# Kernel optimization log

Hardware: AMD Instinct MI355X
Metric: run time of the kernel (lower is better)

Reference implementation:

```python
import jax, jax.numpy as jnp
import numpy as np

B, S, T = 2048, 32, 32
D, H = 128, 256       # cle_dim, rnn_dim
VS, VT = 256, 256     # source/target char vocab
BOW = 1               # MorphoDataset.Factor.BOW


def setup_inputs() -> dict:
    key = jax.random.key(0)
    ks = jax.random.split(key, 16)
    n = lambda k, sh: (jax.random.normal(k, sh, jnp.float32) * 0.05)
    inp = {
        "src_emb": n(ks[0], (VS, D)),
        "tgt_emb": n(ks[1], (VT, D)),
        "enc_f_W": n(ks[2], (D, 3 * H)),
        "enc_f_U": n(ks[3], (H, 3 * H)),
        "enc_f_b": jnp.zeros((2, 3 * H), jnp.float32),
        "enc_b_W": n(ks[4], (D, 3 * H)),
        "enc_b_U": n(ks[5], (H, 3 * H)),
        "enc_b_b": jnp.zeros((2, 3 * H), jnp.float32),
        "dec_W": n(ks[6], (D + H, 3 * H)),
        "dec_U": n(ks[7], (H, 3 * H)),
        "dec_b": jnp.zeros((2, 3 * H), jnp.float32),
        "out_W": n(ks[8], (H, VT)),
        "out_b": jnp.zeros((VT,), jnp.float32),
        "att_src_W": n(ks[9], (H, H)),
        "att_src_b": jnp.zeros((H,), jnp.float32),
        "att_st_W": n(ks[10], (H, H)),
        "att_st_b": jnp.zeros((H,), jnp.float32),
        "att_v": n(ks[11], (H, 1)),
        "att_v_b": jnp.zeros((1,), jnp.float32),
        "source_ids": jax.random.randint(ks[12], (B, S), 0, VS, jnp.int32),
        "target_ids": jax.random.randint(ks[13], (B, T), 0, VT, jnp.int32),
    }
    return inp


def _gru_step(h, x, W, U, b):
    # Keras GRU, reset_after=True: separate input/recurrent biases b[0], b[1]
    gx = x @ W + b[0]
    gh = h @ U + b[1]
    xz, xr, xh = jnp.split(gx, 3, axis=-1)
    hz, hr, hh = jnp.split(gh, 3, axis=-1)
    z = jax.nn.sigmoid(xz + hz)
    r = jax.nn.sigmoid(xr + hr)
    c = jnp.tanh(xh + r * hh)
    return z * h + (1.0 - z) * c


def _gru_scan(x_tbd, W, U, b):
    # x_tbd: [S, B, D] -> outputs [S, B, H]
    h0 = jnp.zeros((x_tbd.shape[1], U.shape[0]), x_tbd.dtype)
    def step(h, x):
        h = _gru_step(h, x, W, U, b)
        return h, h
    _, ys = jax.lax.scan(step, h0, x_tbd)
    return ys


def reference(src_emb, tgt_emb, enc_f_W, enc_f_U, enc_f_b, enc_b_W, enc_b_U, enc_b_b,
              dec_W, dec_U, dec_b, out_W, out_b, att_src_W, att_src_b,
              att_st_W, att_st_b, att_v, att_v_b, source_ids, target_ids):
    # ---- Encoder: bidirectional GRU, merge_mode='sum' ----
    x = src_emb[source_ids]                      # [B, S, D]
    x_t = jnp.transpose(x, (1, 0, 2))            # [S, B, D]
    fwd = _gru_scan(x_t, enc_f_W, enc_f_U, enc_f_b)
    bwd = _gru_scan(x_t[::-1], enc_b_W, enc_b_U, enc_b_b)[::-1]
    source_states = jnp.transpose(fwd + bwd, (1, 0, 2))  # [B, S, H]

    # projected source states are constant across decoder steps -> precompute
    proj_src = source_states @ att_src_W + att_src_b     # [B, S, H]

    def attend(inp, h):
        p = h @ att_st_W + att_st_b                      # [B, H]
        e = jnp.tanh(proj_src + p[:, None, :]) @ att_v + att_v_b  # [B, S, 1]
        w = jax.nn.softmax(e, axis=1)                    # softmax over source positions
        ctx = jnp.sum(source_states * w, axis=1)         # [B, H]
        return jnp.concatenate([inp, ctx], axis=1)       # [B, D+H]

    # ---- Decoder (teacher forcing) ----
    h0 = source_states[:, 0]                             # [B, H]
    bow = jnp.broadcast_to(tgt_emb[BOW], (source_ids.shape[0], tgt_emb.shape[1]))
    inp0 = attend(bow, h0)

    def dstep(carry, tgt_t):
        h, inp = carry
        h = _gru_step(h, inp, dec_W, dec_U, dec_b)       # GRUCell step
        logits = h @ out_W + out_b                       # [B, VT]
        nxt = attend(tgt_emb[tgt_t], h)
        return (h, nxt), logits

    _, logits = jax.lax.scan(dstep, (h0, inp0), jnp.transpose(target_ids))
    return jnp.transpose(logits, (1, 0, 2))              # [B, T, VT]
```

## Files before the change

### kernel.cpp

```cpp
#include <hip/hip_runtime.h>
#include <math.h>

#define B_  2048
#define S_  32
#define T_  32
#define D_  128
#define H_  256
#define G3  768
#define VT_ 256
#define BOW_ 1

typedef __attribute__((ext_vector_type(8))) short short8;
typedef __attribute__((ext_vector_type(4))) float f32x4;
typedef __attribute__((ext_vector_type(8))) unsigned short us8;
typedef unsigned short u16;

__device__ inline u16 f2bf(float x) {
  union { float f; unsigned u; } v; v.f = x;
  unsigned r = v.u + 0x7FFFu + ((v.u >> 16) & 1u);
  return (u16)(r >> 16);
}
__device__ inline float bf2f(u16 b) {
  union { unsigned u; float f; } v; v.u = ((unsigned)b) << 16; return v.f;
}
__device__ inline int swz(int r) { return ((r ^ (r >> 3)) & 7) << 3; }
__device__ inline float sigm(float x) { return 1.f / (1.f + expf(-x)); }

struct TMat { const float* src; u16* dhi; u16* dlo; int R; int C; int tile0; };
struct TPack { TMat m[10]; };

__global__ __launch_bounds__(256)
void wsplit_t(TPack P) {
  int bx = blockIdx.x;
  TMat M = P.m[0];
  #pragma unroll
  for (int i = 1; i < 10; i++) if (bx >= P.m[i].tile0) M = P.m[i];
  int ti = bx - M.tile0;
  int tilesR = M.R >> 6;
  int rt = ti % tilesR, ct = ti / tilesR;
  int r0 = rt * 64, c0 = ct * 64;
  __shared__ float ts[64][65];
  int tid = threadIdx.x;
  int cx = tid & 63, ry = tid >> 6;
  #pragma unroll
  for (int i = 0; i < 16; i++) {
    int r = ry * 16 + i;
    ts[r][cx] = M.src[(size_t)(r0 + r) * M.C + c0 + cx];
  }
  __syncthreads();
  int rx = tid & 63, cy = tid >> 6;
  #pragma unroll
  for (int i = 0; i < 16; i++) {
    int cc = cy * 16 + i;
    float v = ts[rx][cc];
    u16 hi = f2bf(v);
    size_t o = (size_t)(c0 + cc) * M.R + r0 + rx;
    M.dhi[o] = hi;
    M.dlo[o] = f2bf(v - bf2f(hi));
  }
}

__global__ __launch_bounds__(256)
void esplit(const float* a, const float* b, u16* ah, u16* al, u16* bh, u16* bl, int n) {
  int i = blockIdx.x * 256 + threadIdx.x;
  if (i >= 2 * n) return;
  const float* s = (i < n) ? a : b;
  u16* dh = (i < n) ? ah : bh;
  u16* dl = (i < n) ? al : bl;
  int j = (i < n) ? i : i - n;
  float v = s[j];
  u16 hi = f2bf(v);
  dh[j] = hi; dl[j] = f2bf(v - bf2f(hi));
}

struct PLeg {
  const u16* Ahi; const u16* Alo; int lda;
  const u16* Bthi; const u16* Btlo; int ldb;
  const float* bias; void* C; int ldc; int cmode;
  int M, N, K;
};

__global__ __launch_bounds__(256)
void gemm_pl(PLeg l0, PLeg l1) {
  PLeg L = blockIdx.z ? l1 : l0;
  int n0 = blockIdx.x * 128; if (n0 >= L.N) return;
  int m0 = blockIdx.y * 128; if (m0 >= L.M) return;
  __shared__ u16 As[128 * 64];
  __shared__ u16 Bs[128 * 64];
  int tid = threadIdx.x;
  int lane = tid & 63, wv = tid >> 6;
  int wr = (wv >> 1) * 64, wc = (wv & 1) * 64;
  int fr = lane & 15, fk = (lane >> 4) * 8;
  f32x4 acc[4][4];
  #pragma unroll
  for (int m = 0; m < 4; m++)
    #pragma unroll
    for (int n = 0; n < 4; n++) acc[m][n] = (f32x4){0.f, 0.f, 0.f, 0.f};

  int s_row = tid >> 1, s_part = tid & 1;

  for (int k0 = 0; k0 < L.K; k0 += 32) {
    if (k0) __syncthreads();
    int swA = swz(s_row);
    {
      const u16* src = (s_part ? L.Alo : L.Ahi) + (size_t)(m0 + s_row) * L.lda + k0;
      #pragma unroll
      for (int q = 0; q < 4; q++)
        *(us8*)&As[(s_row * 64 + s_part * 32 + q * 8) ^ swA] = *(const us8*)(src + q * 8);
    }
    {
      const u16* src = (s_part ? L.Btlo : L.Bthi) + (size_t)(n0 + s_row) * L.ldb + k0;
      #pragma unroll
      for (int q = 0; q < 4; q++)
        *(us8*)&Bs[(s_row * 64 + s_part * 32 + q * 8) ^ swA] = *(const us8*)(src + q * 8);
    }
    __syncthreads();
    short8 bhi[4], blo[4];
    #pragma unroll
    for (int n = 0; n < 4; n++) {
      int cc = wc + n * 16 + fr; int sw = swz(cc);
      bhi[n] = *(const short8*)&Bs[(cc * 64 + fk) ^ sw];
      blo[n] = *(const short8*)&Bs[(cc * 64 + 32 + fk) ^ sw];
    }
    #pragma unroll
    for (int m = 0; m < 4; m++) {
      int r = wr + m * 16 + fr; int sw = swz(r);
      short8 ahi = *(const short8*)&As[(r * 64 + fk) ^ sw];
      short8 alo = *(const short8*)&As[(r * 64 + 32 + fk) ^ sw];
      #pragma unroll
      for (int n = 0; n < 4; n++) {
        acc[m][n] = __builtin_amdgcn_mfma_f32_16x16x32_bf16(ahi, bhi[n], acc[m][n], 0, 0, 0);
        acc[m][n] = __builtin_amdgcn_mfma_f32_16x16x32_bf16(ahi, blo[n], acc[m][n], 0, 0, 0);
        acc[m][n] = __builtin_amdgcn_mfma_f32_16x16x32_bf16(alo, bhi[n], acc[m][n], 0, 0, 0);
      }
    }
  }
  int rbase = (lane >> 4) * 4;
  #pragma unroll
  for (int m = 0; m < 4; m++)
    #pragma unroll
    for (int rr = 0; rr < 4; rr++) {
      int row = m0 + wr + m * 16 + rbase + rr;
      #pragma unroll
      for (int n = 0; n < 4; n++) {
        int col = n0 + wc + n * 16 + fr;
        float v = acc[m][n][rr];
        if (L.bias) v += L.bias[col];
        if (L.cmode == 0)      ((float*)L.C)[(size_t)row * L.ldc + col] = v;
        else if (L.cmode == 1) ((u16*)L.C)[(size_t)row * L.ldc + col] = f2bf(v);
        else {
          size_t o = (((size_t)(row & (B_ - 1))) * T_ + (row >> 11)) * VT_ + col;
          ((float*)L.C)[o] = v;
        }
      }
    }
}

struct GruDesc {
  const u16 *a0H, *a0L;
  const u16 *a1H, *a1L;
  const u16 *b0H, *b0L;
  const u16 *b1H, *b1L;
  const float *gxT;
  const float *bias0, *bias1;
  const float *hold;
  const u16 *holdH, *holdL;
  float *hnew;
  u16 *hh, *hl;
  u16 *ssH, *ssL;
  const int *ids;
  int ssmode;
  int sidx, rev;
};

template<int MODE>
__global__ __launch_bounds__(256)
void gru_step(GruDesc d0, GruDesc d1) {
  GruDesc D = blockIdx.z ? d1 : d0;
  constexpr int KT  = MODE ? 512 : 256;
  constexpr int KT8 = KT / 8;
  constexpr int MF  = MODE ? 1 : 2;
  constexpr int NST = KT / 32;
  __shared__ __align__(16) u16 As[2 * 32 * KT];

  int m0 = blockIdx.y * 32;
  int tid = threadIdx.x;
  int lane = tid & 63, wv = tid >> 6;
  int fr = lane & 15, kq = lane >> 4;
  int jn, rb0;
  if (MODE == 0) { jn = blockIdx.x * 64 + wv * 16 + fr; rb0 = 0; }
  else           { jn = blockIdx.x * 32 + (wv & 1) * 16 + fr; rb0 = (wv >> 1) * 16; }

  constexpr int PER_T = (2 * 32 * KT8) / 256;
  #pragma unroll
  for (int i = 0; i < PER_T; i++) {
    int s = tid + i * 256;
    int p = s / (32 * KT8);
    int rem = s - p * (32 * KT8);
    int row = rem / KT8;
    int kb = rem - row * KT8;
    int k = kb * 8;
    const u16* src;
    if (MODE == 0) {
      src = (p ? D.a0L : D.a0H) + (size_t)(m0 + row) * 256 + k;
    } else {
      src = (k < 256) ? (p ? D.a0L : D.a0H) + (size_t)(m0 + row) * 256 + k
                      : (p ? D.a1L : D.a1H) + (size_t)(m0 + row) * 256 + (k - 256);
    }
    *(us8*)&As[(s ^ (row & 7)) * 8] = *(const us8*)src;
  }
  __syncthreads();

  f32x4 acc[4][MF];
  #pragma unroll
  for (int a = 0; a < 4; a++)
    #pragma unroll
    for (int mf = 0; mf < MF; mf++) acc[a][mf] = (f32x4){0.f, 0.f, 0.f, 0.f};

  #pragma unroll
  for (int i = 0; i < NST; i++) {
    const u16 *BH, *BL; int bk, ai2;
    if (MODE == 0)    { BH = D.b0H; BL = D.b0L; bk = i * 32; ai2 = 2; }
    else if (i < 8)   { BH = D.b0H; BL = D.b0L; bk = i * 32; ai2 = 2; }
    else              { BH = D.b1H; BL = D.b1L; bk = (i - 8) * 32; ai2 = 3; }
    short8 ah[MF], al[MF];
    #pragma unroll
    for (int mf = 0; mf < MF; mf++) {
      int rp = rb0 + mf * 16 + fr;
      int kb = i * 4 + kq;
      ah[mf] = *(const short8*)&As[((rp * KT8 + kb) ^ (fr & 7)) * 8];
      al[mf] = *(const short8*)&As[((32 * KT8 + rp * KT8 + kb) ^ (fr & 7)) * 8];
    }
    #pragma unroll
    for (int st = 0; st < 3; st++) {
      size_t ro = (size_t)(st * 256 + jn) * 256 + bk + kq * 8;
      short8 bh = *(const short8*)(BH + ro);
      short8 bl = *(const short8*)(BL + ro);
      int ai = (st < 2) ? st : ai2;
      #pragma unroll
      for (int mf = 0; mf < MF; mf++) {
        acc[ai][mf] = __builtin_amdgcn_mfma_f32_16x16x32_bf16(ah[mf], bh, acc[ai][mf], 0, 0, 0);
        acc[ai][mf] = __builtin_amdgcn_mfma_f32_16x16x32_bf16(ah[mf], bl, acc[ai][mf], 0, 0, 0);
        acc[ai][mf] = __builtin_amdgcn_mfma_f32_16x16x32_bf16(al[mf], bh, acc[ai][mf], 0, 0, 0);
      }
    }
  }

  int rbase = kq * 4;
  int j = jn;
  float b0z = D.bias0[j],       b1z = D.bias1[j];
  float b0r = D.bias0[256 + j], b1r = D.bias1[256 + j];
  float b0c = D.bias0[512 + j], b1c = D.bias1[512 + j];
  #pragma unroll
  for (int mf = 0; mf < MF; mf++)
    #pragma unroll
    for (int rr = 0; rr < 4; rr++) {
      int b = m0 + rb0 + mf * 16 + rbase + rr;
      size_t o = (size_t)b * H_ + j;
      int id;
      if (MODE == 0) id = D.ids[b * S_ + (D.rev ? (S_ - 1 - D.sidx) : D.sidx)];
      else           id = (D.sidx == 0) ? BOW_ : D.ids[b * T_ + D.sidx - 1];
      const float* T = D.gxT + (size_t)id * G3;
      float z = sigm(acc[0][mf][rr] + T[j] + b0z + b1z);
      float r = sigm(acc[1][mf][rr] + T[256 + j] + b0r + b1r);
      float xc = T[512 + j] + b0c + (MODE ? acc[3][mf][rr] : 0.f);
      float c = tanhf(xc + r * (acc[2][mf][rr] + b1c));
      float hprev = D.hold ? D.hold[o] : (bf2f(D.holdH[o]) + bf2f(D.holdL[o]));
      float hn = z * hprev + (1.f - z) * c;
      D.hnew[o] = hn;
      u16 hi = f2bf(hn);
      D.hh[o] = hi; D.hl[o] = f2bf(hn - bf2f(hi));
      if (MODE == 0) {
        if (D.ssmode == 1) {
          D.ssH[o] = hi; D.ssL[o] = f2bf(hn - bf2f(hi));
        } else if (D.ssmode == 2) {
          float v = bf2f(D.ssH[o]) + bf2f(D.ssL[o]) + hn;
          u16 vh = f2bf(v);
          D.ssH[o] = vh; D.ssL[o] = f2bf(v - bf2f(vh));
        }
      }
    }
}

__global__ __launch_bounds__(256)
void attend_k(const u16* __restrict__ projbf, const u16* __restrict__ ssH,
              const float* __restrict__ p, const float* __restrict__ att_v,
              u16* __restrict__ ctxh, u16* __restrict__ ctxl) {
  int b = blockIdx.x;
  int tid = threadIdx.x;
  int lane = tid & 63;
  int wv = tid >> 6;
  __shared__ float e_s[S_];
  __shared__ float w_s[S_];
  float pq[4], vq[4];
  #pragma unroll
  for (int q = 0; q < 4; q++) {
    pq[q] = p[(size_t)b * H_ + q * 64 + lane];
    vq[q] = att_v[q * 64 + lane];
  }
  float pv[8][4];
  #pragma unroll
  for (int i = 0; i < 8; i++) {
    const u16* pr = projbf + ((size_t)(wv * 8 + i) * B_ + b) * H_;
    #pragma unroll
    for (int q = 0; q < 4; q++) pv[i][q] = bf2f(pr[q * 64 + lane]);
  }
  u16 sv[S_];
  #pragma unroll
  for (int s = 0; s < S_; s++) sv[s] = ssH[((size_t)s * B_ + b) * H_ + tid];

  #pragma unroll
  for (int i = 0; i < 8; i++) {
    float part = 0.f;
    #pragma unroll
    for (int q = 0; q < 4; q++)
      part += tanhf(pv[i][q] + pq[q]) * vq[q];
    #pragma unroll
    for (int off = 32; off; off >>= 1)
      part += __shfl_xor(part, off);
    if (lane == 0) e_s[wv * 8 + i] = part;
  }
  __syncthreads();
  float m = -1e30f;
  #pragma unroll
  for (int s = 0; s < S_; s++) m = fmaxf(m, e_s[s]);
  float den = 0.f;
  #pragma unroll
  for (int s = 0; s < S_; s++) den += expf(e_s[s] - m);
  if (tid < S_) w_s[tid] = expf(e_s[tid] - m) / den;
  __syncthreads();
  float acc = 0.f;
  #pragma unroll
  for (int s = 0; s < S_; s++)
    acc = fmaf(w_s[s], bf2f(sv[s]), acc);
  u16 hi = f2bf(acc);
  size_t o = (size_t)b * H_ + tid;
  ctxh[o] = hi; ctxl[o] = f2bf(acc - bf2f(hi));
}

extern "C" void kernel_launch(void* const* d_in, const int* in_sizes, int n_in,
                              void* d_out, int out_size, void* d_ws, size_t ws_size,
                              hipStream_t stream) {
  const float* src_emb   = (const float*)d_in[0];
  const float* tgt_emb   = (const float*)d_in[1];
  const float* enc_f_W   = (const float*)d_in[2];
  const float* enc_f_U   = (const float*)d_in[3];
  const float* enc_f_b   = (const float*)d_in[4];
  const float* enc_b_W   = (const float*)d_in[5];
  const float* enc_b_U   = (const float*)d_in[6];
  const float* enc_b_b   = (const float*)d_in[7];
  const float* dec_W     = (const float*)d_in[8];
  const float* dec_U     = (const float*)d_in[9];
  const float* dec_b     = (const float*)d_in[10];
  const float* out_W     = (const float*)d_in[11];
  const float* out_b     = (const float*)d_in[12];
  const float* att_src_W = (const float*)d_in[13];
  const float* att_src_b = (const float*)d_in[14];
  const float* att_st_W  = (const float*)d_in[15];
  const float* att_st_b  = (const float*)d_in[16];
  const float* att_v     = (const float*)d_in[17];
  const int* source_ids  = (const int*)d_in[19];
  const int* target_ids  = (const int*)d_in[20];
  float* out = (float*)d_out;

  char* base = (char*)d_ws;
  size_t off = 0;
  auto allocB = [&](size_t bytes) { void* p = base + off; off = (off + bytes + 255) & ~255UL; return p; };
  const size_t BH = (size_t)B_ * H_;

  u16* ssH    = (u16*)allocB((size_t)S_ * BH * 2);
  u16* ssL    = (u16*)allocB((size_t)S_ * BH * 2);
  u16* projbf = (u16*)allocB((size_t)S_ * BH * 2);
  float* pbuf = (float*)allocB(BH * 4);
  u16* ctxh = (u16*)allocB(BH * 2);
  u16* ctxl = (u16*)allocB(BH * 2);

  float* encF0 = (float*)allocB(2 * BH * 4);
  u16*  encPl0 = (u16*)allocB(4 * BH * 2);
  float* encF1 = (float*)allocB(2 * BH * 4);
  u16*  encPl1 = (u16*)allocB(4 * BH * 2);
  float* encF[2][2]  = { { encF0, encF0 + BH }, { encF1, encF1 + BH } };
  u16*  encH[2][2]   = { { encPl0, encPl0 + 2 * BH }, { encPl1, encPl1 + 2 * BH } };
  u16*  encL[2][2]   = { { encPl0 + BH, encPl0 + 3 * BH }, { encPl1 + BH, encPl1 + 3 * BH } };

  float* hDecF[2] = { (float*)allocB(BH * 4), (float*)allocB(BH * 4) };
  u16* hAllH = (u16*)allocB((size_t)T_ * BH * 2);
  u16* hAllL = (u16*)allocB((size_t)T_ * BH * 2);

  auto planes2 = [&](size_t n, u16*& h, u16*& l) { h = (u16*)allocB(n * 2); l = (u16*)allocB(n * 2); };
  u16 *UtFh,*UtFl,*UtBh,*UtBl,*WtFh,*WtFl,*WtBh,*WtBl;
  u16 *dUth,*dUtl,*dWcth,*dWctl,*dWxth,*dWxtl;
  u16 *oWth,*oWtl,*aStth,*aSttl,*aSrth,*aSrtl;
  u16 *sEh,*sEl,*tEh,*tEl;
  planes2((size_t)G3*H_, UtFh, UtFl);   planes2((size_t)G3*H_, UtBh, UtBl);
  planes2((size_t)G3*D_, WtFh, WtFl);   planes2((size_t)G3*D_, WtBh, WtBl);
  planes2((size_t)G3*H_, dUth, dUtl);   planes2((size_t)G3*H_, dWcth, dWctl);
  planes2((size_t)G3*D_, dWxth, dWxtl);
  planes2((size_t)H_*VT_, oWth, oWtl);
  planes2((size_t)H_*H_, aSrth, aSrtl);
  planes2((size_t)H_*H_, aStth, aSttl);
  planes2((size_t)VT_*D_, sEh, sEl);    planes2((size_t)VT_*D_, tEh, tEl);
  float* Tf = (float*)allocB((size_t)VT_ * G3 * 4);
  float* Tb = (float*)allocB((size_t)VT_ * G3 * 4);
  float* Td = (float*)allocB((size_t)VT_ * G3 * 4);

  TPack P;
  P.m[0] = { enc_f_U,          UtFh, UtFl, 256, 768, 0   };
  P.m[1] = { enc_b_U,          UtBh, UtBl, 256, 768, 48  };
  P.m[2] = { dec_U,            dUth, dUtl, 256, 768, 96  };
  P.m[3] = { dec_W + 128 * G3, dWcth, dWctl, 256, 768, 144 };
  P.m[4] = { enc_f_W,          WtFh, WtFl, 128, 768, 192 };
  P.m[5] = { enc_b_W,          WtBh, WtBl, 128, 768, 216 };
  P.m[6] = { dec_W,            dWxth, dWxtl, 128, 768, 240 };
  P.m[7] = { out_W,            oWth, oWtl, 256, 256, 264 };
  P.m[8] = { att_src_W,        aSrth, aSrtl, 256, 256, 280 };
  P.m[9] = { att_st_W,         aStth, aSttl, 256, 256, 296 };
  wsplit_t<<<312, 256, 0, stream>>>(P);
  esplit<<<(2 * VT_ * D_ + 255) / 256, 256, 0, stream>>>(src_emb, tgt_emb, sEh, sEl, tEh, tEl, VT_ * D_);

  {
    PLeg tf = { sEh, sEl, D_, WtFh, WtFl, D_, nullptr, Tf, G3, 0, VT_, G3, D_ };
    PLeg tb = { sEh, sEl, D_, WtBh, WtBl, D_, nullptr, Tb, G3, 0, VT_, G3, D_ };
    gemm_pl<<<dim3(6, 2, 2), 256, 0, stream>>>(tf, tb);
    PLeg td = { tEh, tEl, D_, dWxth, dWxtl, D_, nullptr, Td, G3, 0, VT_, G3, D_ };
    gemm_pl<<<dim3(6, 2, 1), 256, 0, stream>>>(td, td);
  }

  hipMemsetAsync(encF0, 0, 2 * BH * 4, stream);
  hipMemsetAsync(encPl0, 0, 4 * BH * 2, stream);

  for (int s = 0; s < S_; s++) {
    int p = s & 1;
    GruDesc dd[2];
    for (int d = 0; d < 2; d++) {
      GruDesc& D = dd[d];
      D.a0H = encH[p][d]; D.a0L = encL[p][d];
      D.a1H = nullptr; D.a1L = nullptr;
      D.b0H = d ? UtBh : UtFh; D.b0L = d ? UtBl : UtFl;
      D.b1H = nullptr; D.b1L = nullptr;
      D.gxT = d ? Tb : Tf;
      D.bias0 = d ? enc_b_b : enc_f_b;
      D.bias1 = (d ? enc_b_b : enc_f_b) + G3;
      D.hold = encF[p][d]; D.holdH = nullptr; D.holdL = nullptr;
      D.hnew = encF[p ^ 1][d];
      D.hh = encH[p ^ 1][d]; D.hl = encL[p ^ 1][d];
      int pos = d ? (S_ - 1 - s) : s;
      D.ssH = ssH + (size_t)pos * BH; D.ssL = ssL + (size_t)pos * BH;
      D.ids = source_ids;
      D.ssmode = (s < S_ / 2) ? 1 : 2;
      D.sidx = s; D.rev = d;
    }
    gru_step<0><<<dim3(4, 64, 2), 256, 0, stream>>>(dd[0], dd[1]);
  }

  {
    PLeg proj = { ssH, ssL, H_, aSrth, aSrtl, H_, att_src_b, projbf, H_, 1, S_ * B_, H_, H_ };
    PLeg p0   = { ssH, ssL, H_, aStth, aSttl, H_, att_st_b,  pbuf,   H_, 0, B_,      H_, H_ };
    gemm_pl<<<dim3(2, 512, 2), 256, 0, stream>>>(proj, p0);
  }
  attend_k<<<B_, 256, 0, stream>>>(projbf, ssH, pbuf, att_v, ctxh, ctxl);

  for (int t = 0; t < T_; t++) {
    int p = t & 1;
    GruDesc D = {};
    D.a0H = t ? hAllH + (size_t)(t - 1) * BH : ssH;
    D.a0L = t ? hAllL + (size_t)(t - 1) * BH : ssL;
    D.a1H = ctxh; D.a1L = ctxl;
    D.b0H = dUth;  D.b0L = dUtl;
    D.b1H = dWcth; D.b1L = dWctl;
    D.gxT = Td;
    D.bias0 = dec_b; D.bias1 = dec_b + G3;
    if (t == 0) { D.hold = nullptr; D.holdH = ssH; D.holdL = ssL; }
    else        { D.hold = hDecF[p]; D.holdH = nullptr; D.holdL = nullptr; }
    D.hnew = hDecF[p ^ 1];
    D.hh = hAllH + (size_t)t * BH; D.hl = hAllL + (size_t)t * BH;
    D.ssH = nullptr; D.ssL = nullptr;
    D.ids = target_ids;
    D.ssmode = 0; D.sidx = t; D.rev = 0;
    gru_step<1><<<dim3(8, 64, 1), 256, 0, stream>>>(D, D);

    if (t < T_ - 1) {
      PLeg LP = { hAllH + (size_t)t * BH, hAllL + (size_t)t * BH, H_,
                  aStth, aSttl, H_, att_st_b, pbuf, H_, 0, B_, H_, H_ };
      gemm_pl<<<dim3(2, 16, 1), 256, 0, stream>>>(LP, LP);
      attend_k<<<B_, 256, 0, stream>>>(projbf, ssH, pbuf, att_v, ctxh, ctxl);
    }
  }

  {
    PLeg LO = { hAllH, hAllL, H_, oWth, oWtl, H_, out_b, out, 0, 2, T_ * B_, VT_, H_ };
    gemm_pl<<<dim3(2, 512, 1), 256, 0, stream>>>(LO, LO);
  }
}
```

Baseline: 3.604 ms.

## Fuse decoder GRU step, attention projection and attention into one kernel

Replaces the per-timestep decoder sequence of GRU kernel, state-projection GEMM and attention kernel with a single dec_step kernel. Each 512-thread block owns 8 batch rows: it computes the GRU update, projects the new state through att_st_W, and computes the attention context, with intermediates kept in shared memory. This removes two launches per step and the global round trip of the projected state. In exchange, every block streams the full recurrent and attention weights, and the 8-row tiles are padded to the 16-row MFMA shape, so half of the matrix work is wasted. The encoder GRU kernel is also specialised into its own non-templated version with fixed indexing.

```diff
diff --git a/kernel.cpp b/kernel.cpp
--- a/kernel.cpp
+++ b/kernel.cpp
@@ -14,6 +14,8 @@
 typedef __attribute__((ext_vector_type(4))) float f32x4;
 typedef __attribute__((ext_vector_type(8))) unsigned short us8;
 typedef unsigned short u16;
+
+#define MFMA16 __builtin_amdgcn_mfma_f32_16x16x32_bf16
 
 __device__ inline u16 f2bf(float x) {
   union { float f; unsigned u; } v; v.f = x;
@@ -129,9 +131,9 @@
       short8 alo = *(const short8*)&As[(r * 64 + 32 + fk) ^ sw];
       #pragma unroll
       for (int n = 0; n < 4; n++) {
-        acc[m][n] = __builtin_amdgcn_mfma_f32_16x16x32_bf16(ahi, bhi[n], acc[m][n], 0, 0, 0);
-        acc[m][n] = __builtin_amdgcn_mfma_f32_16x16x32_bf16(ahi, blo[n], acc[m][n], 0, 0, 0);
-        acc[m][n] = __builtin_amdgcn_mfma_f32_16x16x32_bf16(alo, bhi[n], acc[m][n], 0, 0, 0);
+        acc[m][n] = MFMA16(ahi, bhi[n], acc[m][n], 0, 0, 0);
+        acc[m][n] = MFMA16(ahi, blo[n], acc[m][n], 0, 0, 0);
+        acc[m][n] = MFMA16(alo, bhi[n], acc[m][n], 0, 0, 0);
       }
     }
   }
@@ -156,15 +158,12 @@
     }
 }
 
-struct GruDesc {
+struct EncD {
   const u16 *a0H, *a0L;
-  const u16 *a1H, *a1L;
   const u16 *b0H, *b0L;
-  const u16 *b1H, *b1L;
   const float *gxT;
   const float *bias0, *bias1;
   const float *hold;
-  const u16 *holdH, *holdL;
   float *hnew;
   u16 *hh, *hl;
   u16 *ssH, *ssL;
@@ -173,111 +172,89 @@
   int sidx, rev;
 };
 
-template<int MODE>
 __global__ __launch_bounds__(256)
-void gru_step(GruDesc d0, GruDesc d1) {
-  GruDesc D = blockIdx.z ? d1 : d0;
-  constexpr int KT  = MODE ? 512 : 256;
-  constexpr int KT8 = KT / 8;
-  constexpr int MF  = MODE ? 1 : 2;
-  constexpr int NST = KT / 32;
-  __shared__ __align__(16) u16 As[2 * 32 * KT];
+void enc_step(EncD d0, EncD d1) {
+  EncD D = blockIdx.z ? d1 : d0;
+  __shared__ __align__(16) u16 As[2 * 32 * 256];
 
   int m0 = blockIdx.y * 32;
   int tid = threadIdx.x;
   int lane = tid & 63, wv = tid >> 6;
   int fr = lane & 15, kq = lane >> 4;
-  int jn, rb0;
-  if (MODE == 0) { jn = blockIdx.x * 64 + wv * 16 + fr; rb0 = 0; }
-  else           { jn = blockIdx.x * 32 + (wv & 1) * 16 + fr; rb0 = (wv >> 1) * 16; }
-
-  constexpr int PER_T = (2 * 32 * KT8) / 256;
-  #pragma unroll
-  for (int i = 0; i < PER_T; i++) {
+  int jn = blockIdx.x * 64 + wv * 16 + fr;
+
+  #pragma unroll
+  for (int i = 0; i < 8; i++) {
     int s = tid + i * 256;
-    int p = s / (32 * KT8);
-    int rem = s - p * (32 * KT8);
-    int row = rem / KT8;
-    int kb = rem - row * KT8;
-    int k = kb * 8;
-    const u16* src;
-    if (MODE == 0) {
-      src = (p ? D.a0L : D.a0H) + (size_t)(m0 + row) * 256 + k;
-    } else {
-      src = (k < 256) ? (p ? D.a0L : D.a0H) + (size_t)(m0 + row) * 256 + k
-                      : (p ? D.a1L : D.a1H) + (size_t)(m0 + row) * 256 + (k - 256);
-    }
+    int p = s >> 10;
+    int rem = s & 1023;
+    int row = rem >> 5;
+    const u16* src = (p ? D.a0L : D.a0H) + (size_t)(m0 + row) * 256 + (rem & 31) * 8;
     *(us8*)&As[(s ^ (row & 7)) * 8] = *(const us8*)src;
   }
   __syncthreads();
 
-  f32x4 acc[4][MF];
-  #pragma unroll
-  for (int a = 0; a < 4; a++)
-    #pragma unroll
-    for (int mf = 0; mf < MF; mf++) acc[a][mf] = (f32x4){0.f, 0.f, 0.f, 0.f};
-
-  #pragma unroll
-  for (int i = 0; i < NST; i++) {
-    const u16 *BH, *BL; int bk, ai2;
-    if (MODE == 0)    { BH = D.b0H; BL = D.b0L; bk = i * 32; ai2 = 2; }
-    else if (i < 8)   { BH = D.b0H; BL = D.b0L; bk = i * 32; ai2 = 2; }
-    else              { BH = D.b1H; BL = D.b1L; bk = (i - 8) * 32; ai2 = 3; }
-    short8 ah[MF], al[MF];
-    #pragma unroll
-    for (int mf = 0; mf < MF; mf++) {
-      int rp = rb0 + mf * 16 + fr;
+  f32x4 acc[3];
+  #pragma unroll
+  for (int a = 0; a < 3; a++) acc[a] = (f32x4){0.f,0.f,0.f,0.f};
+  f32x4 acc2[3];
+  #pragma unroll
+  for (int a = 0; a < 3; a++) acc2[a] = (f32x4){0.f,0.f,0.f,0.f};
+
+  #pragma unroll
+  for (int i = 0; i < 8; i++) {
+    short8 ah[2], al[2];
+    #pragma unroll
+    for (int mf = 0; mf < 2; mf++) {
+      int rp = mf * 16 + fr;
       int kb = i * 4 + kq;
-      ah[mf] = *(const short8*)&As[((rp * KT8 + kb) ^ (fr & 7)) * 8];
-      al[mf] = *(const short8*)&As[((32 * KT8 + rp * KT8 + kb) ^ (fr & 7)) * 8];
+      ah[mf] = *(const short8*)&As[((rp * 32 + kb) ^ (fr & 7)) * 8];
+      al[mf] = *(const short8*)&As[((1024 + rp * 32 + kb) ^ (fr & 7)) * 8];
     }
     #pragma unroll
     for (int st = 0; st < 3; st++) {
-      size_t ro = (size_t)(st * 256 + jn) * 256 + bk + kq * 8;
-      short8 bh = *(const short8*)(BH + ro);
-      short8 bl = *(const short8*)(BL + ro);
-      int ai = (st < 2) ? st : ai2;
-      #pragma unroll
-      for (int mf = 0; mf < MF; mf++) {
-        acc[ai][mf] = __builtin_amdgcn_mfma_f32_16x16x32_bf16(ah[mf], bh, acc[ai][mf], 0, 0, 0);
-        acc[ai][mf] = __builtin_amdgcn_mfma_f32_16x16x32_bf16(ah[mf], bl, acc[ai][mf], 0, 0, 0);
-        acc[ai][mf] = __builtin_amdgcn_mfma_f32_16x16x32_bf16(al[mf], bh, acc[ai][mf], 0, 0, 0);
-      }
-    }
-  }
-
+      size_t ro = (size_t)(st * 256 + jn) * 256 + i * 32 + kq * 8;
+      short8 bh = *(const short8*)(D.b0H + ro);
+      short8 bl = *(const short8*)(D.b0L + ro);
+      acc[st]  = MFMA16(ah[0], bh, acc[st], 0, 0, 0);
+      acc[st]  = MFMA16(ah[0], bl, acc[st], 0, 0, 0);
+      acc[st]  = MFMA16(al[0], bh, acc[st], 0, 0, 0);
+      acc2[st] = MFMA16(ah[1], bh, acc2[st], 0, 0, 0);
+      acc2[st] = MFMA16(ah[1], bl, acc2[st], 0, 0, 0);
+      acc2[st] = MFMA16(al[1], bh, acc2[st], 0, 0, 0);
+    }
+  }
+
+  float b0z = D.bias0[jn] + D.bias1[jn];
+  float b0r = D.bias0[256 + jn] + D.bias1[256 + jn];
+  float bxc = D.bias0[512 + jn];
+  float bhc = D.bias1[512 + jn];
   int rbase = kq * 4;
-  int j = jn;
-  float b0z = D.bias0[j],       b1z = D.bias1[j];
-  float b0r = D.bias0[256 + j], b1r = D.bias1[256 + j];
-  float b0c = D.bias0[512 + j], b1c = D.bias1[512 + j];
-  #pragma unroll
-  for (int mf = 0; mf < MF; mf++)
+  #pragma unroll
+  for (int mf = 0; mf < 2; mf++)
     #pragma unroll
     for (int rr = 0; rr < 4; rr++) {
-      int b = m0 + rb0 + mf * 16 + rbase + rr;
-      size_t o = (size_t)b * H_ + j;
-      int id;
-      if (MODE == 0) id = D.ids[b * S_ + (D.rev ? (S_ - 1 - D.sidx) : D.sidx)];
-      else           id = (D.sidx == 0) ? BOW_ : D.ids[b * T_ + D.sidx - 1];
+      int b = m0 + mf * 16 + rbase + rr;
+      size_t o = (size_t)b * H_ + jn;
+      int id = D.ids[b * S_ + (D.rev ? (S_ - 1 - D.sidx) : D.sidx)];
       const float* T = D.gxT + (size_t)id * G3;
-      float z = sigm(acc[0][mf][rr] + T[j] + b0z + b1z);
-      float r = sigm(acc[1][mf][rr] + T[256 + j] + b0r + b1r);
-      float xc = T[512 + j] + b0c + (MODE ? acc[3][mf][rr] : 0.f);
-      float c = tanhf(xc + r * (acc[2][mf][rr] + b1c));
-      float hprev = D.hold ? D.hold[o] : (bf2f(D.holdH[o]) + bf2f(D.holdL[o]));
-      float hn = z * hprev + (1.f - z) * c;
+      float az  = mf ? acc2[0][rr] : acc[0][rr];
+      float ar  = mf ? acc2[1][rr] : acc[1][rr];
+      float ahc = mf ? acc2[2][rr] : acc[2][rr];
+      float z = sigm(az + T[jn] + b0z);
+      float r = sigm(ar + T[256 + jn] + b0r);
+      float c = tanhf(T[512 + jn] + bxc + r * (ahc + bhc));
+      float hn = z * D.hold[o] + (1.f - z) * c;
       D.hnew[o] = hn;
       u16 hi = f2bf(hn);
-      D.hh[o] = hi; D.hl[o] = f2bf(hn - bf2f(hi));
-      if (MODE == 0) {
-        if (D.ssmode == 1) {
-          D.ssH[o] = hi; D.ssL[o] = f2bf(hn - bf2f(hi));
-        } else if (D.ssmode == 2) {
-          float v = bf2f(D.ssH[o]) + bf2f(D.ssL[o]) + hn;
-          u16 vh = f2bf(v);
-          D.ssH[o] = vh; D.ssL[o] = f2bf(v - bf2f(vh));
-        }
+      u16 lo = f2bf(hn - bf2f(hi));
+      D.hh[o] = hi; D.hl[o] = lo;
+      if (D.ssmode == 1) {
+        D.ssH[o] = hi; D.ssL[o] = lo;
+      } else {
+        float v = bf2f(D.ssH[o]) + bf2f(D.ssL[o]) + hn;
+        u16 vh = f2bf(v);
+        D.ssH[o] = vh; D.ssL[o] = f2bf(v - bf2f(vh));
       }
     }
 }
@@ -336,6 +313,195 @@
   u16 hi = f2bf(acc);
   size_t o = (size_t)b * H_ + tid;
   ctxh[o] = hi; ctxl[o] = f2bf(acc - bf2f(hi));
+}
+
+struct DSP {
+  const u16 *hPH, *hPL;
+  const float *hPF;
+  float *hFo;
+  const u16 *UH, *UL, *CH, *CL;
+  const u16 *sWH, *sWL;
+  const float *gxT, *bias, *stb, *attv;
+  const u16 *ssH;
+  const u16 *projbf;
+  u16 *hAH, *hAL;
+  u16 *ctxH, *ctxL;
+  const int *ids;
+  int t, last;
+};
+
+__global__ __launch_bounds__(512, 1)
+void dec_step(DSP P) {
+  __shared__ __align__(16) u16 AH[16 * 512];
+  __shared__ __align__(16) u16 AL[16 * 512];
+  __shared__ float pS[8 * 256];
+  const int tid = threadIdx.x;
+  const int lane = tid & 63, w = tid >> 6;
+  const int fr = lane & 15, kq = lane >> 4;
+  const int r0 = blockIdx.x * 8;
+
+  #pragma unroll
+  for (int i = 0; i < 4; i++) {
+    int s = tid + i * 512;
+    int p = s >> 10;
+    int rem = s & 1023;
+    int row = rem >> 6;
+    int k8 = rem & 63;
+    us8 v = {0,0,0,0,0,0,0,0};
+    if (row < 8) {
+      const u16* src = (k8 < 32)
+        ? (p ? P.hPL : P.hPH) + (size_t)(r0 + row) * 256 + k8 * 8
+        : (p ? P.ctxL : P.ctxH) + (size_t)(r0 + row) * 256 + (k8 - 32) * 8;
+      v = *(const us8*)src;
+    }
+    int slot = row * 64 + (k8 ^ (row & 7));
+    if (p) *(us8*)&AL[slot * 8] = v;
+    else   *(us8*)&AH[slot * 8] = v;
+  }
+  __syncthreads();
+
+  f32x4 acc[4][2];
+  #pragma unroll
+  for (int a = 0; a < 4; a++)
+    #pragma unroll
+    for (int q = 0; q < 2; q++) acc[a][q] = (f32x4){0.f,0.f,0.f,0.f};
+
+  #pragma unroll
+  for (int i = 0; i < 16; i++) {
+    int slot = fr * 64 + ((i * 4 + kq) ^ (fr & 7));
+    short8 ah = *(const short8*)&AH[slot * 8];
+    short8 al = *(const short8*)&AL[slot * 8];
+    const u16* BH = (i < 8) ? P.UH : P.CH;
+    const u16* BL = (i < 8) ? P.UL : P.CL;
+    int bk = (i & 7) * 32 + kq * 8;
+    int ci = (i < 8) ? 2 : 3;
+    #pragma unroll
+    for (int st = 0; st < 3; st++) {
+      int ai = (st < 2) ? st : ci;
+      #pragma unroll
+      for (int q = 0; q < 2; q++) {
+        size_t ro = (size_t)(st * 256 + (2 * w + q) * 16 + fr) * 256 + bk;
+        short8 bh = *(const short8*)(BH + ro);
+        short8 bl = *(const short8*)(BL + ro);
+        acc[ai][q] = MFMA16(ah, bh, acc[ai][q], 0, 0, 0);
+        acc[ai][q] = MFMA16(ah, bl, acc[ai][q], 0, 0, 0);
+        acc[ai][q] = MFMA16(al, bh, acc[ai][q], 0, 0, 0);
+      }
+    }
+  }
+  __syncthreads();
+
+  if (kq < 2) {
+    #pragma unroll
+    for (int rr = 0; rr < 4; rr++) {
+      int row = kq * 4 + rr;
+      int gb = r0 + row;
+      int id = (P.t == 0) ? BOW_ : P.ids[gb * T_ + P.t - 1];
+      const float* T = P.gxT + (size_t)id * G3;
+      #pragma unroll
+      for (int q = 0; q < 2; q++) {
+        int j = (2 * w + q) * 16 + fr;
+        size_t o = (size_t)gb * H_ + j;
+        float z = sigm(acc[0][q][rr] + T[j] + P.bias[j] + P.bias[G3 + j]);
+        float r = sigm(acc[1][q][rr] + T[256 + j] + P.bias[256 + j] + P.bias[G3 + 256 + j]);
+        float c = tanhf(T[512 + j] + P.bias[512 + j] + acc[3][q][rr]
+                        + r * (acc[2][q][rr] + P.bias[G3 + 512 + j]));
+        float hp;
+        if (P.hPF) hp = P.hPF[o];
+        else {
+          int sl = row * 64 + ((j >> 3) ^ (row & 7));
+          hp = bf2f(AH[sl * 8 + (j & 7)]) + bf2f(AL[sl * 8 + (j & 7)]);
+        }
+        float hn = z * hp + (1.f - z) * c;
+        P.hFo[o] = hn;
+        u16 hi = f2bf(hn);
+        u16 lo = f2bf(hn - bf2f(hi));
+        P.hAH[o] = hi; P.hAL[o] = lo;
+        int sl = row * 64 + ((j >> 3) ^ (row & 7));
+        AH[sl * 8 + (j & 7)] = hi;
+        AL[sl * 8 + (j & 7)] = lo;
+      }
+    }
+  }
+  if (P.last) return;
+  __syncthreads();
+
+  f32x4 pa[2];
+  #pragma unroll
+  for (int q = 0; q < 2; q++) pa[q] = (f32x4){0.f,0.f,0.f,0.f};
+  #pragma unroll
+  for (int i = 0; i < 8; i++) {
+    int slot = fr * 64 + ((i * 4 + kq) ^ (fr & 7));
+    short8 ah = *(const short8*)&AH[slot * 8];
+    short8 al = *(const short8*)&AL[slot * 8];
+    #pragma unroll
+    for (int q = 0; q < 2; q++) {
+      size_t ro = (size_t)((2 * w + q) * 16 + fr) * 256 + i * 32 + kq * 8;
+      short8 bh = *(const short8*)(P.sWH + ro);
+      short8 bl = *(const short8*)(P.sWL + ro);
+      pa[q] = MFMA16(ah, bh, pa[q], 0, 0, 0);
+      pa[q] = MFMA16(ah, bl, pa[q], 0, 0, 0);
+      pa[q] = MFMA16(al, bh, pa[q], 0, 0, 0);
+    }
+  }
+  if (kq < 2) {
+    #pragma unroll
+    for (int rr = 0; rr < 4; rr++) {
+      int row = kq * 4 + rr;
+      #pragma unroll
+      for (int q = 0; q < 2; q++) {
+        int j = (2 * w + q) * 16 + fr;
+        pS[row * 256 + j] = pa[q][rr] + P.stb[j];
+      }
+    }
+  }
+  __syncthreads();
+
+  {
+    int gb = r0 + w;
+    float pq[4], vq[4];
+    #pragma unroll
+    for (int q = 0; q < 4; q++) {
+      pq[q] = pS[w * 256 + q * 64 + lane];
+      vq[q] = P.attv[q * 64 + lane];
+    }
+    float sc[S_];
+    #pragma unroll 8
+    for (int s2 = 0; s2 < S_; s2++) {
+      const u16* pr = P.projbf + ((size_t)s2 * B_ + gb) * 256;
+      float part = 0.f;
+      #pragma unroll
+      for (int q = 0; q < 4; q++)
+        part += tanhf(bf2f(pr[q * 64 + lane]) + pq[q]) * vq[q];
+      #pragma unroll
+      for (int off = 32; off; off >>= 1)
+        part += __shfl_xor(part, off);
+      sc[s2] = part;
+    }
+    float m = -1e30f;
+    #pragma unroll
+    for (int s2 = 0; s2 < S_; s2++) m = fmaxf(m, sc[s2]);
+    float den = 0.f;
+    #pragma unroll
+    for (int s2 = 0; s2 < S_; s2++) { sc[s2] = expf(sc[s2] - m); den += sc[s2]; }
+    float inv = 1.f / den;
+    float cacc[4] = {0.f, 0.f, 0.f, 0.f};
+    #pragma unroll 8
+    for (int s2 = 0; s2 < S_; s2++) {
+      float wgt = sc[s2] * inv;
+      const u16* sp = P.ssH + ((size_t)s2 * B_ + gb) * 256;
+      #pragma unroll
+      for (int q = 0; q < 4; q++)
+        cacc[q] = fmaf(wgt, bf2f(sp[q * 64 + lane]), cacc[q]);
+    }
+    #pragma unroll
+    for (int q = 0; q < 4; q++) {
+      size_t o = (size_t)gb * H_ + q * 64 + lane;
+      u16 hi = f2bf(cacc[q]);
+      P.ctxH[o] = hi;
+      P.ctxL[o] = f2bf(cacc[q] - bf2f(hi));
+    }
+  }
 }
 
 extern "C" void kernel_launch(void* const* d_in, const int* in_sizes, int n_in,
@@ -431,17 +597,15 @@
 
   for (int s = 0; s < S_; s++) {
     int p = s & 1;
-    GruDesc dd[2];
+    EncD dd[2];
     for (int d = 0; d < 2; d++) {
-      GruDesc& D = dd[d];
+      EncD& D = dd[d];
       D.a0H = encH[p][d]; D.a0L = encL[p][d];
-      D.a1H = nullptr; D.a1L = nullptr;
       D.b0H = d ? UtBh : UtFh; D.b0L = d ? UtBl : UtFl;
-      D.b1H = nullptr; D.b1L = nullptr;
       D.gxT = d ? Tb : Tf;
       D.bias0 = d ? enc_b_b : enc_f_b;
       D.bias1 = (d ? enc_b_b : enc_f_b) + G3;
-      D.hold = encF[p][d]; D.holdH = nullptr; D.holdL = nullptr;
+      D.hold = encF[p][d];
       D.hnew = encF[p ^ 1][d];
       D.hh = encH[p ^ 1][d]; D.hl = encL[p ^ 1][d];
       int pos = d ? (S_ - 1 - s) : s;
@@ -450,7 +614,7 @@
       D.ssmode = (s < S_ / 2) ? 1 : 2;
       D.sidx = s; D.rev = d;
     }
-    gru_step<0><<<dim3(4, 64, 2), 256, 0, stream>>>(dd[0], dd[1]);
+    enc_step<<<dim3(4, 64, 2), 256, 0, stream>>>(dd[0], dd[1]);
   }
 
   {
@@ -461,30 +625,21 @@
   attend_k<<<B_, 256, 0, stream>>>(projbf, ssH, pbuf, att_v, ctxh, ctxl);
 
   for (int t = 0; t < T_; t++) {
-    int p = t & 1;
-    GruDesc D = {};
-    D.a0H = t ? hAllH + (size_t)(t - 1) * BH : ssH;
-    D.a0L = t ? hAllL + (size_t)(t - 1) * BH : ssL;
-    D.a1H = ctxh; D.a1L = ctxl;
-    D.b0H = dUth;  D.b0L = dUtl;
-    D.b1H = dWcth; D.b1L = dWctl;
-    D.gxT = Td;
-    D.bias0 = dec_b; D.bias1 = dec_b + G3;
-    if (t == 0) { D.hold = nullptr; D.holdH = ssH; D.holdL = ssL; }
-    else        { D.hold = hDecF[p]; D.holdH = nullptr; D.holdL = nullptr; }
-    D.hnew = hDecF[p ^ 1];
-    D.hh = hAllH + (size_t)t * BH; D.hl = hAllL + (size_t)t * BH;
-    D.ssH = nullptr; D.ssL = nullptr;
+    DSP D;
+    D.hPH = t ? hAllH + (size_t)(t - 1) * BH : ssH;
+    D.hPL = t ? hAllL + (size_t)(t - 1) * BH : ssL;
+    D.hPF = t ? hDecF[t & 1] : nullptr;
+    D.hFo = hDecF[(t & 1) ^ 1];
+    D.UH = dUth; D.UL = dUtl; D.CH = dWcth; D.CL = dWctl;
+    D.sWH = aStth; D.sWL = aSttl;
+    D.gxT = Td; D.bias = dec_b; D.stb = att_st_b; D.attv = att_v;
+    D.ssH = ssH;
+    D.projbf = projbf;
+    D.hAH = hAllH + (size_t)t * BH; D.hAL = hAllL + (size_t)t * BH;
+    D.ctxH = ctxh; D.ctxL = ctxl;
     D.ids = target_ids;
-    D.ssmode = 0; D.sidx = t; D.rev = 0;
-    gru_step<1><<<dim3(8, 64, 1), 256, 0, stream>>>(D, D);
-
-    if (t < T_ - 1) {
-      PLeg LP = { hAllH + (size_t)t * BH, hAllL + (size_t)t * BH, H_,
-                  aStth, aSttl, H_, att_st_b, pbuf, H_, 0, B_, H_, H_ };
-      gemm_pl<<<dim3(2, 16, 1), 256, 0, stream>>>(LP, LP);
-      attend_k<<<B_, 256, 0, stream>>>(projbf, ssH, pbuf, att_v, ctxh, ctxl);
-    }
+    D.t = t; D.last = (t == T_ - 1) ? 1 : 0;
+    dec_step<<<256, 512, 0, stream>>>(D);
   }
 
   {
```

Measured after the change: 4.294 ms. +19.2%, slower.
